# Kernel tuning notes

Hardware: AMD Instinct MI355X
Metric: run time of the kernel (lower is better)

Reference implementation:

```python
import jax, jax.numpy as jnp
import numpy as np

N_MEMORY, N_LOOPS, N_LATENT = 1067, 8, 128
N_CONTEXT = 64
MAX_FEAT = N_LOOPS * N_CONTEXT * N_LATENT  # 65536
BLOCK = 2048


def setup_inputs() -> dict:
    key = jax.random.key(0)
    ks = jax.random.split(key, 10)
    return {
        "memory": jax.random.normal(ks[0], (N_MEMORY, N_LOOPS, N_LATENT), jnp.float32),
        "z_in": jax.random.normal(ks[1], (N_LATENT,), jnp.float32),
        # scale weights so the F=65536 matvec output stays O(1)
        "weights": jax.random.normal(ks[2], (N_LOOPS, MAX_FEAT, N_LATENT), jnp.float32) * 0.005,
        "center": jax.random.normal(ks[3], (N_LOOPS, MAX_FEAT), jnp.float32),
        "bias": jax.random.normal(ks[4], (N_LOOPS, N_LATENT), jnp.float32),
        "z_min": jax.random.normal(ks[5], (N_LOOPS, N_LATENT), jnp.float32) - 2.0,
        "z_max": jax.random.normal(ks[6], (N_LOOPS, N_LATENT), jnp.float32) + 2.0,
        "limit_margin": jax.random.uniform(ks[7], (N_LATENT,), jnp.float32),
        "mask": jax.random.uniform(ks[8], (2, N_LOOPS), jnp.float32),
        "y_audio": jax.random.normal(ks[9], (N_LOOPS, 1, BLOCK), jnp.float32),
        "record_index": 500,
        "active_loop": 3,       # 1-indexed, as in LivingLooper.forward
        "latency_correct": 2,
        "context": N_CONTEXT,
    }


def _target_process_inv(z):
    # torch.where(z>1, 2*z**0.5 - 1, where(z<-1, 1 - 2*(-z)**0.5, z)); safe sqrt for jax where
    hi = 2.0 * jnp.sqrt(jnp.maximum(z, 1.0)) - 1.0
    lo = 1.0 - 2.0 * jnp.sqrt(jnp.maximum(-z, 1.0))
    return jnp.where(z > 1.0, hi, jnp.where(z < -1.0, lo, z))


def reference(memory, z_in, weights, center, bias, z_min, z_max,
              limit_margin, mask, y_audio, record_index, active_loop,
              latency_correct, context):
    n_memory, n_loops, n_latent = memory.shape
    i_act = active_loop - 1

    # --- ring-buffer record of new latent for active loop at dt = lc..0 ---
    rows = (record_index - np.arange(latency_correct + 1)) % n_memory
    mem1 = memory.at[rows, i_act].set(z_in)

    # --- get_frames(context, skip=1): context frames ending at record_index-1 ---
    widx = (record_index - 1 - context + 1 + np.arange(context)) % n_memory
    window = mem1[widx]                       # [ctx, n_loops, n_latent]
    flat = window.reshape(-1)                 # [F], F = ctx*n_loops*n_latent

    # --- per-loop Loop.eval: feat_process -> matvec -> inv -> clamp ---
    x = jnp.tanh((flat[None, :] - center) * 0.5)          # [L, F]
    z = jnp.einsum('lf,lfd->ld', x, weights) + bias       # [L, D]
    z = _target_process_inv(z)
    z = jnp.clip(z, z_min - limit_margin[None, :], z_max + limit_margin[None, :])

    # --- scatter eval results at record_index for all loops except active ---
    keep = (jnp.arange(n_loops) == i_act)[:, None]
    mem2 = mem1.at[record_index].set(jnp.where(keep, mem1[record_index], z))

    zs = mem2[record_index]                   # [L, D] == get_frames(1)

    # --- masked crossfade on decoded audio ---
    fade = jnp.linspace(0.0, 1.0, y_audio.shape[2])
    m = mask[1][:, None, None] * fade + mask[0][:, None, None] * (1.0 - fade)
    y = y_audio * m                           # [L, 1, block]
    return (y, zs, mem2)
```

## Files before the change

kernel.cpp:

```cpp
#include <hip/hip_runtime.h>

typedef float v4f __attribute__((ext_vector_type(4)));


__global__ __launch_bounds__(256) void ll_main_kernel(
    const float* __restrict__ memory, const float* __restrict__ z_in,
    const float* __restrict__ weights, const float* __restrict__ center,
    const float* __restrict__ mask, const float* __restrict__ y_audio,
    const int* __restrict__ rec_p, const int* __restrict__ act_p,
    const int* __restrict__ lc_p, const int* __restrict__ ctx_p,
    float* __restrict__ partials, float* __restrict__ out_y,
    float* __restrict__ out_mem2,
    int L, int D, int F, int n_memory, int blocksPerLoop, int BLK)
{
    __shared__ float x_lds[256];
    __shared__ float ps[8 * 128];

    const int bid = blockIdx.x;
    const int l = bid / blocksPerLoop;
    const int chunk = bid - l * blocksPerLoop;
    const int f0 = chunk * 256;
    const int tid = threadIdx.x;

    const int rec = *rec_p;
    const int i_act = *act_p - 1;
    const int lc = *lc_p;
    const int ctx = *ctx_p;
    const int LD = L * D;

    {
        const int f = f0 + tid;
        const int c = f / LD;
        const int rem = f - c * LD;
        const int ll = rem / D;
        const int dd = rem - ll * D;
        int row = rec - ctx + c;
        row %= n_memory; if (row < 0) row += n_memory;
        int diff = rec - row; if (diff < 0) diff += n_memory;
        float v = (ll == i_act && diff <= lc)
                      ? z_in[dd]
                      : memory[(size_t)row * LD + rem];
        const float cen = center[(size_t)l * F + f];
        x_lds[tid] = tanhf((v - cen) * 0.5f);
    }
    __syncthreads();

    const int g = tid >> 5;
    const int t = tid & 31;
    const v4f* __restrict__ W = (const v4f*)(weights + ((size_t)l * F + f0) * D);
    v4f acc = (v4f)0.f;
    #pragma unroll 8
    for (int i = 0; i < 32; ++i) {
        const int r = i * 8 + g;
        const float xv = x_lds[r];
        const v4f w = __builtin_nontemporal_load(&W[(size_t)r * 32 + t]);
        acc += xv * w;
    }
    ((v4f*)&ps[g * 128])[t] = acc;
    __syncthreads();

    if (tid < 128) {
        float s = 0.f;
        #pragma unroll
        for (int gg = 0; gg < 8; ++gg) s += ps[gg * 128 + tid];
        partials[(size_t)bid * 128 + tid] = s;
    }

    const int gsize = gridDim.x * 256;
    const int Ncopy = n_memory * LD;
    const int total = Ncopy + L * BLK;
    for (int idx = bid * 256 + tid; idx < total; idx += gsize) {
        if (idx < Ncopy) {
            const int row = idx / LD;
            if (row == rec) continue;
            const int rem = idx - row * LD;
            const int ll = rem / D;
            const int dd = rem - ll * D;
            int diff = rec - row; if (diff < 0) diff += n_memory;
            const float v = (ll == i_act && diff <= lc) ? z_in[dd] : memory[idx];
            __builtin_nontemporal_store(v, &out_mem2[idx]);
        } else {
            const int j = idx - Ncopy;
            const int li = j / BLK;
            const int k = j - li * BLK;
            const float fade = (float)k / (float)(BLK - 1);
            const float m = mask[L + li] * fade + mask[li] * (1.f - fade);
            out_y[j] = y_audio[j] * m;
        }
    }
}

__global__ __launch_bounds__(256) void ll_finalize_kernel(
    const float* __restrict__ partials, const float* __restrict__ bias,
    const float* __restrict__ z_min, const float* __restrict__ z_max,
    const float* __restrict__ limit_margin, const float* __restrict__ z_in,
    const int* __restrict__ rec_p, const int* __restrict__ act_p,
    float* __restrict__ out_zs, float* __restrict__ out_mem2,
    int L, int D, int blocksPerLoop)
{
    const int tid = blockIdx.x * blockDim.x + threadIdx.x;
    if (tid >= L * D) return;
    const int l = tid / D;
    const int d = tid - l * D;

    float s = 0.f;
    const float* __restrict__ p = partials + (size_t)l * blocksPerLoop * D + d;
    #pragma unroll 8
    for (int c = 0; c < blocksPerLoop; ++c)
        s += p[(size_t)c * D];

    float z = s + bias[tid];
    const float hi = 2.f * sqrtf(fmaxf(z, 1.f)) - 1.f;
    const float lo = 1.f - 2.f * sqrtf(fmaxf(-z, 1.f));
    z = (z > 1.f) ? hi : ((z < -1.f) ? lo : z);
    const float zl = z_min[tid] - limit_margin[d];
    const float zh = z_max[tid] + limit_margin[d];
    z = fminf(fmaxf(z, zl), zh);

    const float out = (l == (*act_p - 1)) ? z_in[d] : z;
    out_zs[tid] = out;
    out_mem2[(size_t)(*rec_p) * (L * D) + tid] = out;
}

extern "C" void kernel_launch(void* const* d_in, const int* in_sizes, int n_in,
                              void* d_out, int out_size, void* d_ws, size_t ws_size,
                              hipStream_t stream) {
    const float* memory       = (const float*)d_in[0];
    const float* z_in         = (const float*)d_in[1];
    const float* weights      = (const float*)d_in[2];
    const float* center       = (const float*)d_in[3];
    const float* bias         = (const float*)d_in[4];
    const float* z_min        = (const float*)d_in[5];
    const float* z_max        = (const float*)d_in[6];
    const float* limit_margin = (const float*)d_in[7];
    const float* mask         = (const float*)d_in[8];
    const float* y_audio      = (const float*)d_in[9];
    const int*   rec_p        = (const int*)d_in[10];
    const int*   act_p        = (const int*)d_in[11];
    const int*   lc_p         = (const int*)d_in[12];
    const int*   ctx_p        = (const int*)d_in[13];

    const int D        = in_sizes[1];
    const int L        = in_sizes[4] / D;
    const int LD       = L * D;
    const int n_memory = in_sizes[0] / LD;
    const int F        = in_sizes[3] / L;
    const int BLK      = in_sizes[9] / L;

    float* out_y    = (float*)d_out;
    float* out_zs   = out_y + (size_t)L * BLK;
    float* out_mem2 = out_zs + LD;

    float* partials = (float*)d_ws;

    const int blocksPerLoop = F / 256;
    ll_main_kernel<<<L * blocksPerLoop, 256, 0, stream>>>(
        memory, z_in, weights, center, mask, y_audio,
        rec_p, act_p, lc_p, ctx_p,
        partials, out_y, out_mem2,
        L, D, F, n_memory, blocksPerLoop, BLK);

    ll_finalize_kernel<<<(LD + 255) / 256, 256, 0, stream>>>(
        partials, bias, z_min, z_max, limit_margin, z_in,
        rec_p, act_p, out_zs, out_mem2, L, D, blocksPerLoop);
}
```

Before: 59.53 us.

## Prefetch weights before feature phase, vectorize copies, use shift indexing

Issues the first eight weight loads for each thread before computing the tanh features, so the weight stream overlaps the gather and transcendental phase. The weight access is remapped so each 32-lane group reads a contiguous run of 32 rows, and the nontemporal hint on weight loads is dropped. The memory copy and audio crossfade loops now move four floats per thread, and divides and mods are replaced by shifts and masks that assume power-of-two sizes. The ring-buffer modulo is simplified on the assumption that context is at most the record index plus n_memory.

```diff
diff --git a/kernel.cpp b/kernel.cpp
--- a/kernel.cpp
+++ b/kernel.cpp
@@ -11,81 +11,98 @@
     const int* __restrict__ lc_p, const int* __restrict__ ctx_p,
     float* __restrict__ partials, float* __restrict__ out_y,
     float* __restrict__ out_mem2,
-    int L, int D, int F, int n_memory, int blocksPerLoop, int BLK)
+    int L, int F, int n_memory, int blocksPerLoop, int BLK,
+    int Dsh, int LDsh, int BLKsh)
 {
     __shared__ float x_lds[256];
     __shared__ float ps[8 * 128];
+
+    const int D  = 1 << Dsh;
+    const int LD = 1 << LDsh;
 
     const int bid = blockIdx.x;
     const int l = bid / blocksPerLoop;
     const int chunk = bid - l * blocksPerLoop;
     const int f0 = chunk * 256;
     const int tid = threadIdx.x;
+    const int g = tid >> 5;
+    const int t = tid & 31;
 
     const int rec = *rec_p;
     const int i_act = *act_p - 1;
     const int lc = *lc_p;
     const int ctx = *ctx_p;
-    const int LD = L * D;
+
+    const v4f* __restrict__ Wv =
+        (const v4f*)(weights + (((size_t)(l * F + f0) + (g << 5)) << Dsh)) + t;
+    v4f pre[8];
+    #pragma unroll
+    for (int j = 0; j < 8; ++j) pre[j] = Wv[j << 5];
 
     {
         const int f = f0 + tid;
-        const int c = f / LD;
-        const int rem = f - c * LD;
-        const int ll = rem / D;
-        const int dd = rem - ll * D;
+        const int c = f >> LDsh;
+        const int rem = f & (LD - 1);
+        const int ll = rem >> Dsh;
+        const int dd = rem & (D - 1);
         int row = rec - ctx + c;
-        row %= n_memory; if (row < 0) row += n_memory;
-        int diff = rec - row; if (diff < 0) diff += n_memory;
-        float v = (ll == i_act && diff <= lc)
-                      ? z_in[dd]
-                      : memory[(size_t)row * LD + rem];
+        if (row < 0) row += n_memory;
+        const int dt = ctx - c;
+        const float v = (ll == i_act && dt <= lc)
+                            ? z_in[dd]
+                            : memory[((size_t)row << LDsh) + rem];
         const float cen = center[(size_t)l * F + f];
         x_lds[tid] = tanhf((v - cen) * 0.5f);
     }
     __syncthreads();
 
-    const int g = tid >> 5;
-    const int t = tid & 31;
-    const v4f* __restrict__ W = (const v4f*)(weights + ((size_t)l * F + f0) * D);
     v4f acc = (v4f)0.f;
+    #pragma unroll
+    for (int j = 0; j < 8; ++j) acc += x_lds[(g << 5) + j] * pre[j];
     #pragma unroll 8
-    for (int i = 0; i < 32; ++i) {
-        const int r = i * 8 + g;
-        const float xv = x_lds[r];
-        const v4f w = __builtin_nontemporal_load(&W[(size_t)r * 32 + t]);
-        acc += xv * w;
-    }
-    ((v4f*)&ps[g * 128])[t] = acc;
+    for (int i = 8; i < 32; ++i)
+        acc += x_lds[(g << 5) + i] * Wv[i << 5];
+
+    ((v4f*)&ps[g << 7])[t] = acc;
     __syncthreads();
 
     if (tid < 128) {
         float s = 0.f;
         #pragma unroll
-        for (int gg = 0; gg < 8; ++gg) s += ps[gg * 128 + tid];
-        partials[(size_t)bid * 128 + tid] = s;
+        for (int gg = 0; gg < 8; ++gg) s += ps[(gg << 7) + tid];
+        partials[((size_t)bid << 7) + tid] = s;
     }
 
     const int gsize = gridDim.x * 256;
-    const int Ncopy = n_memory * LD;
-    const int total = Ncopy + L * BLK;
-    for (int idx = bid * 256 + tid; idx < total; idx += gsize) {
-        if (idx < Ncopy) {
-            const int row = idx / LD;
+    const int Ncopy4 = (n_memory << LDsh) >> 2;
+    const int total4 = Ncopy4 + ((L * BLK) >> 2);
+    for (int i4 = bid * 256 + tid; i4 < total4; i4 += gsize) {
+        if (i4 < Ncopy4) {
+            const int idx = i4 << 2;
+            const int row = idx >> LDsh;
             if (row == rec) continue;
-            const int rem = idx - row * LD;
-            const int ll = rem / D;
-            const int dd = rem - ll * D;
+            const int rem = idx & (LD - 1);
+            const int ll = rem >> Dsh;
+            const int dd = rem & (D - 1);
             int diff = rec - row; if (diff < 0) diff += n_memory;
-            const float v = (ll == i_act && diff <= lc) ? z_in[dd] : memory[idx];
-            __builtin_nontemporal_store(v, &out_mem2[idx]);
+            v4f v;
+            if (ll == i_act && diff <= lc) v = *(const v4f*)(z_in + dd);
+            else                           v = *(const v4f*)(memory + idx);
+            __builtin_nontemporal_store(v, (v4f*)(out_mem2 + idx));
         } else {
-            const int j = idx - Ncopy;
-            const int li = j / BLK;
-            const int k = j - li * BLK;
-            const float fade = (float)k / (float)(BLK - 1);
-            const float m = mask[L + li] * fade + mask[li] * (1.f - fade);
-            out_y[j] = y_audio[j] * m;
+            const int j = (i4 - Ncopy4) << 2;
+            const int li = j >> BLKsh;
+            const int k = j & ((1 << BLKsh) - 1);
+            const float inv = 1.f / (float)((1 << BLKsh) - 1);
+            const float m0 = mask[li], m1 = mask[L + li];
+            const v4f ya = *(const v4f*)(y_audio + j);
+            v4f r;
+            #pragma unroll
+            for (int e = 0; e < 4; ++e) {
+                const float fade = (float)(k + e) * inv;
+                r[e] = ya[e] * (m1 * fade + m0 * (1.f - fade));
+            }
+            *(v4f*)(out_y + j) = r;
         }
     }
 }
@@ -104,7 +121,7 @@
     const int d = tid - l * D;
 
     float s = 0.f;
-    const float* __restrict__ p = partials + (size_t)l * blocksPerLoop * D + d;
+    const float* __restrict__ p = partials + ((size_t)l * blocksPerLoop) * D + d;
     #pragma unroll 8
     for (int c = 0; c < blocksPerLoop; ++c)
         s += p[(size_t)c * D];
@@ -147,6 +164,10 @@
     const int F        = in_sizes[3] / L;
     const int BLK      = in_sizes[9] / L;
 
+    const int Dsh   = __builtin_ctz(D);
+    const int LDsh  = __builtin_ctz(LD);
+    const int BLKsh = __builtin_ctz(BLK);
+
     float* out_y    = (float*)d_out;
     float* out_zs   = out_y + (size_t)L * BLK;
     float* out_mem2 = out_zs + LD;
@@ -158,7 +179,7 @@
         memory, z_in, weights, center, mask, y_audio,
         rec_p, act_p, lc_p, ctx_p,
         partials, out_y, out_mem2,
-        L, D, F, n_memory, blocksPerLoop, BLK);
+        L, F, n_memory, blocksPerLoop, BLK, Dsh, LDsh, BLKsh);
 
     ll_finalize_kernel<<<(LD + 255) / 256, 256, 0, stream>>>(
         partials, bias, z_min, z_max, limit_margin, z_in,
```

New measurement: 58.01 us. 1.03x faster.
